# Kernel tuning notes

Hardware: AMD Instinct MI355X
Metric: run time of the kernel (lower is better)

Reference implementation:

```python
import jax, jax.numpy as jnp
import numpy as np

B, S, H = 32, 2048, 1024

def setup_inputs() -> dict:
    key = jax.random.key(0)
    ks = jax.random.split(key, 8)
    scale = 1.0 / np.sqrt(H)
    return {
        "query": jax.random.normal(ks[0], (B, H), jnp.float32),
        "keys": jax.random.normal(ks[1], (B, S, H), jnp.float32),
        "Wa_w": jax.random.uniform(ks[2], (H, H), jnp.float32, -scale, scale),
        "Wa_b": jax.random.uniform(ks[3], (H,), jnp.float32, -scale, scale),
        "Ua_w": jax.random.uniform(ks[4], (H, H), jnp.float32, -scale, scale),
        "Ua_b": jax.random.uniform(ks[5], (H,), jnp.float32, -scale, scale),
        "Va_w": jax.random.uniform(ks[6], (1, H), jnp.float32, -scale, scale),
        "Va_b": jax.random.uniform(ks[7], (1,), jnp.float32, -scale, scale),
    }

def reference(query, keys, Wa_w, Wa_b, Ua_w, Ua_b, Va_w, Va_b):
    # q_proj: [B, H]; k_proj: [B, S, H]  (torch Linear: x @ W^T + b)
    q_proj = query @ Wa_w.T + Wa_b
    k_proj = jnp.einsum("bsh,gh->bsg", keys, Ua_w) + Ua_b
    # scores: [B, S, 1] via thin Va projection of tanh-combined features
    scores = jnp.tanh(q_proj[:, None, :] + k_proj) @ Va_w.T + Va_b
    weights = jax.nn.softmax(scores, axis=1)            # [B, S, 1]
    context = jnp.einsum("bsx,bsh->bxh", weights, keys)  # [B, 1, H]
    return context, weights[:, :, 0]
```

## Files before the change

### kernel.cpp

```cpp
#include <hip/hip_runtime.h>
#include <hip/hip_bf16.h>
#include <stdint.h>

#define B_ 32
#define S_ 2048
#define H_ 1024

typedef __attribute__((ext_vector_type(8))) short short8;
typedef __attribute__((ext_vector_type(4))) float floatx4;

__device__ inline unsigned short f32_bf16(float f) {
    union { float f; unsigned u; } v; v.f = f;
    unsigned u = v.u;
    u += 0x7fff + ((u >> 16) & 1);
    return (unsigned short)(u >> 16);
}

__device__ inline float tanh_fast(float x) {
    float e = __expf(2.0f * x);
    return 1.0f - 2.0f / (e + 1.0f);
}

__global__ void k_zero2(float* a, int na, float* b, int nb) {
    int i = blockIdx.x * 256 + threadIdx.x;
    if (i < na) a[i] = 0.0f;
    else if (i - na < nb) b[i - na] = 0.0f;
}

__global__ void k_cvt_ua(const float* __restrict__ ua, unsigned short* __restrict__ out) {
    int i = (blockIdx.x * 256 + threadIdx.x) * 4;
    float4 f = *(const float4*)(ua + i);
    unsigned lo = f32_bf16(f.x) | ((unsigned)f32_bf16(f.y) << 16);
    unsigned hi = f32_bf16(f.z) | ((unsigned)f32_bf16(f.w) << 16);
    *(uint2*)(out + i) = make_uint2(lo, hi);
}

__global__ void k_qproj(const float* __restrict__ query, const float* __restrict__ Wa_w,
                        const float* __restrict__ Wa_b, const float* __restrict__ Ua_b,
                        float* __restrict__ qsum) {
    int b = blockIdx.x >> 2;
    int g = ((blockIdx.x & 3) << 8) + threadIdx.x;
    const float4* q4 = (const float4*)(query + (size_t)b * H_);
    const float4* w4 = (const float4*)(Wa_w + (size_t)g * H_);
    float acc = 0.0f;
#pragma unroll 4
    for (int h = 0; h < H_ / 4; ++h) {
        float4 a = q4[h], w = w4[h];
        acc += a.x * w.x + a.y * w.y + a.z * w.z + a.w * w.w;
    }
    qsum[b * H_ + g] = acc + Wa_b[g] + Ua_b[g];
}

#define BM 128
#define BN 128
#define BK 32
#define LDA 48

__global__ __launch_bounds__(256, 2) void k_scores(
    const float* __restrict__ keys, const unsigned short* __restrict__ uab,
    const float* __restrict__ qsum, const float* __restrict__ va,
    float* __restrict__ scores)
{
    __shared__ unsigned short Al[BM * LDA];
    __shared__ unsigned short Bl[BN * LDA];

    int bx = blockIdx.x;
    int x  = bx & 7;
    int i  = bx >> 3;
    int tile_m = x * 64 + (i >> 3);
    int nc     = i & 7;
    int m_base = tile_m * BM;
    int b      = m_base >> 11;
    int g0     = nc * BN;

    int tid = threadIdx.x;
    int wid = tid >> 6, lane = tid & 63;
    int wm = wid >> 1, wn = wid & 1;
    int q = lane >> 4, cn = lane & 15;

    const float*          Aptr = keys + (size_t)m_base * H_;
    const unsigned short* Bptr = uab  + (size_t)g0 * H_;

    int ar = tid >> 3;
    int ac = tid & 7;
    int br = tid >> 2;
    int bc = tid & 3;

    floatx4 acc[4][4];
#pragma unroll
    for (int ii = 0; ii < 4; ++ii)
#pragma unroll
        for (int jj = 0; jj < 4; ++jj)
            acc[ii][jj] = (floatx4)(0.0f);

    float4 a0, a1, a2, a3;
    uint4  bv0, bv1;
    {
        int k0 = 0;
        a0 = *(const float4*)(Aptr + (size_t)(ar      ) * H_ + k0 + ac * 4);
        a1 = *(const float4*)(Aptr + (size_t)(ar + 32 ) * H_ + k0 + ac * 4);
        a2 = *(const float4*)(Aptr + (size_t)(ar + 64 ) * H_ + k0 + ac * 4);
        a3 = *(const float4*)(Aptr + (size_t)(ar + 96 ) * H_ + k0 + ac * 4);
        bv0 = *(const uint4*)(Bptr + (size_t)(br      ) * H_ + k0 + bc * 8);
        bv1 = *(const uint4*)(Bptr + (size_t)(br + 64 ) * H_ + k0 + bc * 8);
    }

    for (int kc = 0; kc < H_ / BK; ++kc) {
        __syncthreads();
        {
            unsigned short* p;
            unsigned lo, hi;
            p = Al + (ar      ) * LDA + ac * 4;
            lo = f32_bf16(a0.x) | ((unsigned)f32_bf16(a0.y) << 16);
            hi = f32_bf16(a0.z) | ((unsigned)f32_bf16(a0.w) << 16);
            *(uint2*)p = make_uint2(lo, hi);
            p = Al + (ar + 32 ) * LDA + ac * 4;
            lo = f32_bf16(a1.x) | ((unsigned)f32_bf16(a1.y) << 16);
            hi = f32_bf16(a1.z) | ((unsigned)f32_bf16(a1.w) << 16);
            *(uint2*)p = make_uint2(lo, hi);
            p = Al + (ar + 64 ) * LDA + ac * 4;
            lo = f32_bf16(a2.x) | ((unsigned)f32_bf16(a2.y) << 16);
            hi = f32_bf16(a2.z) | ((unsigned)f32_bf16(a2.w) << 16);
            *(uint2*)p = make_uint2(lo, hi);
            p = Al + (ar + 96 ) * LDA + ac * 4;
            lo = f32_bf16(a3.x) | ((unsigned)f32_bf16(a3.y) << 16);
            hi = f32_bf16(a3.z) | ((unsigned)f32_bf16(a3.w) << 16);
            *(uint2*)p = make_uint2(lo, hi);
            *(uint4*)(Bl + (br      ) * LDA + bc * 8) = bv0;
            *(uint4*)(Bl + (br + 64 ) * LDA + bc * 8) = bv1;
        }
        if (kc + 1 < H_ / BK) {
            int k0 = (kc + 1) * BK;
            a0 = *(const float4*)(Aptr + (size_t)(ar      ) * H_ + k0 + ac * 4);
            a1 = *(const float4*)(Aptr + (size_t)(ar + 32 ) * H_ + k0 + ac * 4);
            a2 = *(const float4*)(Aptr + (size_t)(ar + 64 ) * H_ + k0 + ac * 4);
            a3 = *(const float4*)(Aptr + (size_t)(ar + 96 ) * H_ + k0 + ac * 4);
            bv0 = *(const uint4*)(Bptr + (size_t)(br      ) * H_ + k0 + bc * 8);
            bv1 = *(const uint4*)(Bptr + (size_t)(br + 64 ) * H_ + k0 + bc * 8);
        }
        __syncthreads();
        short8 af[4], bf[4];
#pragma unroll
        for (int ii = 0; ii < 4; ++ii)
            af[ii] = *(const short8*)(Al + (wm * 64 + ii * 16 + cn) * LDA + q * 8);
#pragma unroll
        for (int jj = 0; jj < 4; ++jj)
            bf[jj] = *(const short8*)(Bl + (wn * 64 + jj * 16 + cn) * LDA + q * 8);
#pragma unroll
        for (int ii = 0; ii < 4; ++ii)
#pragma unroll
            for (int jj = 0; jj < 4; ++jj)
                acc[ii][jj] = __builtin_amdgcn_mfma_f32_16x16x32_bf16(
                    af[ii], bf[jj], acc[ii][jj], 0, 0, 0);
    }

    float qs[4], vw[4];
#pragma unroll
    for (int jj = 0; jj < 4; ++jj) {
        int g = g0 + wn * 64 + jj * 16 + cn;
        qs[jj] = qsum[b * H_ + g];
        vw[jj] = va[g];
    }
#pragma unroll
    for (int ii = 0; ii < 4; ++ii) {
        float rs[4] = {0.f, 0.f, 0.f, 0.f};
#pragma unroll
        for (int jj = 0; jj < 4; ++jj) {
#pragma unroll
            for (int r = 0; r < 4; ++r)
                rs[r] += vw[jj] * tanh_fast(qs[jj] + acc[ii][jj][r]);
        }
#pragma unroll
        for (int r = 0; r < 4; ++r) {
            for (int mm = 1; mm < 16; mm <<= 1)
                rs[r] += __shfl_xor(rs[r], mm);
        }
        if (cn == 0) {
            int msrow = m_base + wm * 64 + ii * 16 + q * 4;
            float* sp = scores + b * S_ + (msrow & (S_ - 1));
            atomicAdd(sp + 0, rs[0]);
            atomicAdd(sp + 1, rs[1]);
            atomicAdd(sp + 2, rs[2]);
            atomicAdd(sp + 3, rs[3]);
        }
    }
}

__global__ void k_softmax(const float* __restrict__ scores, float* __restrict__ weights) {
    int b = blockIdx.x;
    int t = threadIdx.x;
    __shared__ float red[4];
    float v[8];
    float mx = -1e30f;
#pragma unroll
    for (int k = 0; k < 8; ++k) { v[k] = scores[b * S_ + t + k * 256]; mx = fmaxf(mx, v[k]); }
    for (int mm = 1; mm < 64; mm <<= 1) mx = fmaxf(mx, __shfl_xor(mx, mm));
    if ((t & 63) == 0) red[t >> 6] = mx;
    __syncthreads();
    mx = fmaxf(fmaxf(red[0], red[1]), fmaxf(red[2], red[3]));
    float sum = 0.0f;
#pragma unroll
    for (int k = 0; k < 8; ++k) { v[k] = __expf(v[k] - mx); sum += v[k]; }
    for (int mm = 1; mm < 64; mm <<= 1) sum += __shfl_xor(sum, mm);
    __syncthreads();
    if ((t & 63) == 0) red[t >> 6] = sum;
    __syncthreads();
    sum = red[0] + red[1] + red[2] + red[3];
    float inv = 1.0f / sum;
#pragma unroll
    for (int k = 0; k < 8; ++k) weights[b * S_ + t + k * 256] = v[k] * inv;
}

__global__ void k_context(const float* __restrict__ keys, const float* __restrict__ weights,
                          float* __restrict__ ctx) {
    int blk = blockIdx.x;
    int b  = blk >> 5;
    int sc = blk & 31;
    int t  = threadIdx.x;
    const float4* kp = (const float4*)(keys + (size_t)(b * S_ + sc * 64) * H_);
    const float*  wp = weights + b * S_ + sc * 64;
    float4 acc = {0.f, 0.f, 0.f, 0.f};
#pragma unroll 4
    for (int s = 0; s < 64; ++s) {
        float w = wp[s];
        float4 k4 = kp[(size_t)s * (H_ / 4) + t];
        acc.x += w * k4.x; acc.y += w * k4.y; acc.z += w * k4.z; acc.w += w * k4.w;
    }
    float* cp = ctx + b * H_ + t * 4;
    atomicAdd(cp + 0, acc.x); atomicAdd(cp + 1, acc.y);
    atomicAdd(cp + 2, acc.z); atomicAdd(cp + 3, acc.w);
}

extern "C" void kernel_launch(void* const* d_in, const int* in_sizes, int n_in,
                              void* d_out, int out_size, void* d_ws, size_t ws_size,
                              hipStream_t stream) {
    const float* query = (const float*)d_in[0];
    const float* keys  = (const float*)d_in[1];
    const float* Wa_w  = (const float*)d_in[2];
    const float* Wa_b  = (const float*)d_in[3];
    const float* Ua_w  = (const float*)d_in[4];
    const float* Ua_b  = (const float*)d_in[5];
    const float* Va_w  = (const float*)d_in[6];

    float* out     = (float*)d_out;
    float* ctx     = out;
    float* weights = out + B_ * H_;

    char* ws = (char*)d_ws;
    unsigned short* uab   = (unsigned short*)ws;
    float*          qsum  = (float*)(ws + 2u * 1024 * 1024);
    float*          scores= (float*)(ws + 2u * 1024 * 1024 + 128 * 1024);

    k_zero2  <<<(B_ * H_ + B_ * S_ + 255) / 256, 256, 0, stream>>>(ctx, B_ * H_, scores, B_ * S_);
    k_cvt_ua <<<(H_ * H_) / 1024, 256, 0, stream>>>(Ua_w, uab);
    k_qproj  <<<B_ * 4, 256, 0, stream>>>(query, Wa_w, Wa_b, Ua_b, qsum);
    k_scores <<<4096, 256, 0, stream>>>(keys, uab, qsum, Va_w, scores);
    k_softmax<<<B_, 256, 0, stream>>>(scores, weights);
    k_context<<<B_ * 16 * 2, 256, 0, stream>>>(keys, weights, ctx);
}
```

Measured before the change: 636.5 us.

## Pre-convert keys to bf16, use direct-to-LDS loads, restructure qproj and context

```diff
diff --git a/kernel.cpp b/kernel.cpp
--- a/kernel.cpp
+++ b/kernel.cpp
@@ -15,54 +15,99 @@
     u += 0x7fff + ((u >> 16) & 1);
     return (unsigned short)(u >> 16);
 }
+__device__ inline unsigned pack_bf2(float a, float b) {
+    return (unsigned)f32_bf16(a) | ((unsigned)f32_bf16(b) << 16);
+}
+__device__ inline float bf_lo(unsigned u) { union { unsigned u; float f; } v; v.u = u << 16; return v.f; }
+__device__ inline float bf_hi(unsigned u) { union { unsigned u; float f; } v; v.u = u & 0xffff0000u; return v.f; }
 
 __device__ inline float tanh_fast(float x) {
     float e = __expf(2.0f * x);
     return 1.0f - 2.0f / (e + 1.0f);
 }
 
-__global__ void k_zero2(float* a, int na, float* b, int nb) {
-    int i = blockIdx.x * 256 + threadIdx.x;
-    if (i < na) a[i] = 0.0f;
-    else if (i - na < nb) b[i - na] = 0.0f;
-}
-
-__global__ void k_cvt_ua(const float* __restrict__ ua, unsigned short* __restrict__ out) {
-    int i = (blockIdx.x * 256 + threadIdx.x) * 4;
-    float4 f = *(const float4*)(ua + i);
-    unsigned lo = f32_bf16(f.x) | ((unsigned)f32_bf16(f.y) << 16);
-    unsigned hi = f32_bf16(f.z) | ((unsigned)f32_bf16(f.w) << 16);
-    *(uint2*)(out + i) = make_uint2(lo, hi);
+__device__ inline void gld16(const void* g, void* l) {
+    __builtin_amdgcn_global_load_lds(
+        (const __attribute__((address_space(1))) unsigned int*)g,
+        (__attribute__((address_space(3))) unsigned int*)l, 16, 0, 0);
+}
+
+#define KCVT_BLOCKS 32768
+#define UACVT_BLOCKS 512
+#define ZS_BLOCKS 64
+__global__ void k_prep(const float* __restrict__ keys, unsigned short* __restrict__ keysbf,
+                       const float* __restrict__ ua, unsigned short* __restrict__ uab,
+                       float* __restrict__ scores) {
+    int blk = blockIdx.x, t = threadIdx.x;
+    if (blk < KCVT_BLOCKS + UACVT_BLOCKS) {
+        const float* src; unsigned short* dst; size_t base;
+        if (blk < KCVT_BLOCKS) { src = keys; dst = keysbf; base = (size_t)blk * 2048; }
+        else { src = ua; dst = uab; base = (size_t)(blk - KCVT_BLOCKS) * 2048; }
+        float4 v0 = *(const float4*)(src + base + t * 4);
+        float4 v1 = *(const float4*)(src + base + 1024 + t * 4);
+        *(uint2*)(dst + base + t * 4)        = make_uint2(pack_bf2(v0.x, v0.y), pack_bf2(v0.z, v0.w));
+        *(uint2*)(dst + base + 1024 + t * 4) = make_uint2(pack_bf2(v1.x, v1.y), pack_bf2(v1.z, v1.w));
+    } else {
+        int zb = blk - KCVT_BLOCKS - UACVT_BLOCKS;
+        float4 z = {0.f, 0.f, 0.f, 0.f};
+        *(float4*)(scores + zb * 1024 + t * 4) = z;
+    }
 }
 
 __global__ void k_qproj(const float* __restrict__ query, const float* __restrict__ Wa_w,
                         const float* __restrict__ Wa_b, const float* __restrict__ Ua_b,
                         float* __restrict__ qsum) {
-    int b = blockIdx.x >> 2;
-    int g = ((blockIdx.x & 3) << 8) + threadIdx.x;
-    const float4* q4 = (const float4*)(query + (size_t)b * H_);
-    const float4* w4 = (const float4*)(Wa_w + (size_t)g * H_);
-    float acc = 0.0f;
-#pragma unroll 4
-    for (int h = 0; h < H_ / 4; ++h) {
-        float4 a = q4[h], w = w4[h];
-        acc += a.x * w.x + a.y * w.y + a.z * w.z + a.w * w.w;
-    }
-    qsum[b * H_ + g] = acc + Wa_b[g] + Ua_b[g];
+    __shared__ float qs_l[32][68];
+    int g0 = blockIdx.x * 16;
+    int t = threadIdx.x;
+    int r = t >> 4;
+    int l = t & 15;
+    int g = g0 + r;
+    float acc[32];
+#pragma unroll
+    for (int b = 0; b < 32; ++b) acc[b] = 0.0f;
+
+    int sb = t >> 3;
+    int sc = (t & 7) * 8;
+    for (int hc = 0; hc < 16; ++hc) {
+        __syncthreads();
+        float4 v0 = *(const float4*)(query + (size_t)sb * H_ + hc * 64 + sc);
+        float4 v1 = *(const float4*)(query + (size_t)sb * H_ + hc * 64 + sc + 4);
+        *(float4*)&qs_l[sb][sc]     = v0;
+        *(float4*)&qs_l[sb][sc + 4] = v1;
+        __syncthreads();
+        float4 w = *(const float4*)(Wa_w + (size_t)g * H_ + hc * 64 + l * 4);
+#pragma unroll
+        for (int b = 0; b < 32; ++b) {
+            float4 q4 = *(const float4*)&qs_l[b][l * 4];
+            acc[b] += w.x * q4.x + w.y * q4.y + w.z * q4.z + w.w * q4.w;
+        }
+    }
+#pragma unroll
+    for (int b = 0; b < 32; ++b) {
+        float a = acc[b];
+        a += __shfl_xor(a, 1); a += __shfl_xor(a, 2);
+        a += __shfl_xor(a, 4); a += __shfl_xor(a, 8);
+        acc[b] = a;
+    }
+    if (l == 0) {
+        float bias = Wa_b[g] + Ua_b[g];
+#pragma unroll
+        for (int b = 0; b < 32; ++b) qsum[b * H_ + g] = acc[b] + bias;
+    }
 }
 
 #define BM 128
 #define BN 128
 #define BK 32
-#define LDA 48
-
-__global__ __launch_bounds__(256, 2) void k_scores(
-    const float* __restrict__ keys, const unsigned short* __restrict__ uab,
+
+__global__ __launch_bounds__(256, 3) void k_scores(
+    const unsigned short* __restrict__ keysbf, const unsigned short* __restrict__ uab,
     const float* __restrict__ qsum, const float* __restrict__ va,
     float* __restrict__ scores)
 {
-    __shared__ unsigned short Al[BM * LDA];
-    __shared__ unsigned short Bl[BN * LDA];
+    __shared__ unsigned short Al[BM * BK];
+    __shared__ unsigned short Bl[BN * BK];
 
     int bx = blockIdx.x;
     int x  = bx & 7;
@@ -78,13 +123,26 @@
     int wm = wid >> 1, wn = wid & 1;
     int q = lane >> 4, cn = lane & 15;
 
-    const float*          Aptr = keys + (size_t)m_base * H_;
-    const unsigned short* Bptr = uab  + (size_t)g0 * H_;
-
-    int ar = tid >> 3;
-    int ac = tid & 7;
-    int br = tid >> 2;
-    int bc = tid & 3;
+    int rl = lane >> 2, cg = lane & 3;
+    int rA0 = wid * 32 + rl,      rA1 = wid * 32 + 16 + rl;
+    int gA0 = cg ^ ((rA0 >> 1) & 3), gA1 = cg ^ ((rA1 >> 1) & 3);
+    const unsigned short* pA0 = keysbf + (size_t)(m_base + rA0) * H_ + gA0 * 8;
+    const unsigned short* pA1 = keysbf + (size_t)(m_base + rA1) * H_ + gA1 * 8;
+    const unsigned short* pB0 = uab + (size_t)(g0 + rA0) * H_ + gA0 * 8;
+    const unsigned short* pB1 = uab + (size_t)(g0 + rA1) * H_ + gA1 * 8;
+    unsigned short* lA0 = &Al[(wid * 32) * BK];
+    unsigned short* lA1 = &Al[(wid * 32 + 16) * BK];
+    unsigned short* lB0 = &Bl[(wid * 32) * BK];
+    unsigned short* lB1 = &Bl[(wid * 32 + 16) * BK];
+
+    int aoff[4], boff[4];
+#pragma unroll
+    for (int ii = 0; ii < 4; ++ii) {
+        int r = wm * 64 + ii * 16 + cn;
+        aoff[ii] = r * BK + (q ^ ((r >> 1) & 3)) * 8;
+        int rb = wn * 64 + ii * 16 + cn;
+        boff[ii] = rb * BK + (q ^ ((rb >> 1) & 3)) * 8;
+    }
 
     floatx4 acc[4][4];
 #pragma unroll
@@ -93,59 +151,19 @@
         for (int jj = 0; jj < 4; ++jj)
             acc[ii][jj] = (floatx4)(0.0f);
 
-    float4 a0, a1, a2, a3;
-    uint4  bv0, bv1;
-    {
-        int k0 = 0;
-        a0 = *(const float4*)(Aptr + (size_t)(ar      ) * H_ + k0 + ac * 4);
-        a1 = *(const float4*)(Aptr + (size_t)(ar + 32 ) * H_ + k0 + ac * 4);
-        a2 = *(const float4*)(Aptr + (size_t)(ar + 64 ) * H_ + k0 + ac * 4);
-        a3 = *(const float4*)(Aptr + (size_t)(ar + 96 ) * H_ + k0 + ac * 4);
-        bv0 = *(const uint4*)(Bptr + (size_t)(br      ) * H_ + k0 + bc * 8);
-        bv1 = *(const uint4*)(Bptr + (size_t)(br + 64 ) * H_ + k0 + bc * 8);
-    }
-
     for (int kc = 0; kc < H_ / BK; ++kc) {
         __syncthreads();
-        {
-            unsigned short* p;
-            unsigned lo, hi;
-            p = Al + (ar      ) * LDA + ac * 4;
-            lo = f32_bf16(a0.x) | ((unsigned)f32_bf16(a0.y) << 16);
-            hi = f32_bf16(a0.z) | ((unsigned)f32_bf16(a0.w) << 16);
-            *(uint2*)p = make_uint2(lo, hi);
-            p = Al + (ar + 32 ) * LDA + ac * 4;
-            lo = f32_bf16(a1.x) | ((unsigned)f32_bf16(a1.y) << 16);
-            hi = f32_bf16(a1.z) | ((unsigned)f32_bf16(a1.w) << 16);
-            *(uint2*)p = make_uint2(lo, hi);
-            p = Al + (ar + 64 ) * LDA + ac * 4;
-            lo = f32_bf16(a2.x) | ((unsigned)f32_bf16(a2.y) << 16);
-            hi = f32_bf16(a2.z) | ((unsigned)f32_bf16(a2.w) << 16);
-            *(uint2*)p = make_uint2(lo, hi);
-            p = Al + (ar + 96 ) * LDA + ac * 4;
-            lo = f32_bf16(a3.x) | ((unsigned)f32_bf16(a3.y) << 16);
-            hi = f32_bf16(a3.z) | ((unsigned)f32_bf16(a3.w) << 16);
-            *(uint2*)p = make_uint2(lo, hi);
-            *(uint4*)(Bl + (br      ) * LDA + bc * 8) = bv0;
-            *(uint4*)(Bl + (br + 64 ) * LDA + bc * 8) = bv1;
-        }
-        if (kc + 1 < H_ / BK) {
-            int k0 = (kc + 1) * BK;
-            a0 = *(const float4*)(Aptr + (size_t)(ar      ) * H_ + k0 + ac * 4);
-            a1 = *(const float4*)(Aptr + (size_t)(ar + 32 ) * H_ + k0 + ac * 4);
-            a2 = *(const float4*)(Aptr + (size_t)(ar + 64 ) * H_ + k0 + ac * 4);
-            a3 = *(const float4*)(Aptr + (size_t)(ar + 96 ) * H_ + k0 + ac * 4);
-            bv0 = *(const uint4*)(Bptr + (size_t)(br      ) * H_ + k0 + bc * 8);
-            bv1 = *(const uint4*)(Bptr + (size_t)(br + 64 ) * H_ + k0 + bc * 8);
-        }
+        int ko = kc * BK;
+        gld16(pA0 + ko, lA0);
+        gld16(pA1 + ko, lA1);
+        gld16(pB0 + ko, lB0);
+        gld16(pB1 + ko, lB1);
         __syncthreads();
         short8 af[4], bf[4];
 #pragma unroll
-        for (int ii = 0; ii < 4; ++ii)
-            af[ii] = *(const short8*)(Al + (wm * 64 + ii * 16 + cn) * LDA + q * 8);
-#pragma unroll
-        for (int jj = 0; jj < 4; ++jj)
-            bf[jj] = *(const short8*)(Bl + (wn * 64 + jj * 16 + cn) * LDA + q * 8);
+        for (int ii = 0; ii < 4; ++ii) af[ii] = *(const short8*)&Al[aoff[ii]];
+#pragma unroll
+        for (int jj = 0; jj < 4; ++jj) bf[jj] = *(const short8*)&Bl[boff[jj]];
 #pragma unroll
         for (int ii = 0; ii < 4; ++ii)
 #pragma unroll
@@ -211,24 +229,43 @@
     for (int k = 0; k < 8; ++k) weights[b * S_ + t + k * 256] = v[k] * inv;
 }
 
-__global__ void k_context(const float* __restrict__ keys, const float* __restrict__ weights,
-                          float* __restrict__ ctx) {
+__global__ void k_ctx1(const unsigned short* __restrict__ keysbf,
+                       const float* __restrict__ weights, float* __restrict__ partial) {
     int blk = blockIdx.x;
-    int b  = blk >> 5;
-    int sc = blk & 31;
-    int t  = threadIdx.x;
-    const float4* kp = (const float4*)(keys + (size_t)(b * S_ + sc * 64) * H_);
-    const float*  wp = weights + b * S_ + sc * 64;
-    float4 acc = {0.f, 0.f, 0.f, 0.f};
-#pragma unroll 4
-    for (int s = 0; s < 64; ++s) {
-        float w = wp[s];
-        float4 k4 = kp[(size_t)s * (H_ / 4) + t];
-        acc.x += w * k4.x; acc.y += w * k4.y; acc.z += w * k4.z; acc.w += w * k4.w;
-    }
-    float* cp = ctx + b * H_ + t * 4;
-    atomicAdd(cp + 0, acc.x); atomicAdd(cp + 1, acc.y);
-    atomicAdd(cp + 2, acc.z); atomicAdd(cp + 3, acc.w);
+    int b = blk >> 5, sc = blk & 31;
+    int t = threadIdx.x;
+    __shared__ float wl[64];
+    if (t < 64) wl[t] = weights[b * S_ + sc * 64 + t];
+    __syncthreads();
+    const uint4* kp = (const uint4*)(keysbf + (size_t)(b * S_ + sc * 64) * H_);
+    int col = t & 127;
+    int rp  = t >> 7;
+    float a0=0,a1=0,a2=0,a3=0,a4=0,a5=0,a6=0,a7=0;
+#pragma unroll 8
+    for (int s = rp; s < 64; s += 2) {
+        uint4 v = kp[(size_t)s * 128 + col];
+        float w = wl[s];
+        a0 += w * bf_lo(v.x); a1 += w * bf_hi(v.x);
+        a2 += w * bf_lo(v.y); a3 += w * bf_hi(v.y);
+        a4 += w * bf_lo(v.z); a5 += w * bf_hi(v.z);
+        a6 += w * bf_lo(v.w); a7 += w * bf_hi(v.w);
+    }
+    float* pp = partial + (size_t)(b * 64 + sc * 2 + rp) * H_ + col * 8;
+    float4 o0 = {a0, a1, a2, a3}, o1 = {a4, a5, a6, a7};
+    *(float4*)pp = o0;
+    *(float4*)(pp + 4) = o1;
+}
+
+__global__ void k_ctx2(const float* __restrict__ partial, float* __restrict__ ctx) {
+    int b = blockIdx.x;
+    int t = threadIdx.x;
+    float4 a = {0.f, 0.f, 0.f, 0.f};
+#pragma unroll 8
+    for (int j = 0; j < 64; ++j) {
+        float4 p = *(const float4*)(partial + (size_t)(b * 64 + j) * H_ + t * 4);
+        a.x += p.x; a.y += p.y; a.z += p.z; a.w += p.w;
+    }
+    *(float4*)(ctx + b * H_ + t * 4) = a;
 }
 
 extern "C" void kernel_launch(void* const* d_in, const int* in_sizes, int n_in,
@@ -247,14 +284,16 @@
     float* weights = out + B_ * H_;
 
     char* ws = (char*)d_ws;
-    unsigned short* uab   = (unsigned short*)ws;
-    float*          qsum  = (float*)(ws + 2u * 1024 * 1024);
-    float*          scores= (float*)(ws + 2u * 1024 * 1024 + 128 * 1024);
-
-    k_zero2  <<<(B_ * H_ + B_ * S_ + 255) / 256, 256, 0, stream>>>(ctx, B_ * H_, scores, B_ * S_);
-    k_cvt_ua <<<(H_ * H_) / 1024, 256, 0, stream>>>(Ua_w, uab);
-    k_qproj  <<<B_ * 4, 256, 0, stream>>>(query, Wa_w, Wa_b, Ua_b, qsum);
-    k_scores <<<4096, 256, 0, stream>>>(keys, uab, qsum, Va_w, scores);
+    unsigned short* keysbf = (unsigned short*)ws;
+    unsigned short* uab    = (unsigned short*)(ws + 134217728);
+    float*          qsum   = (float*)(ws + 134217728 + 2097152);
+    float*          scores = (float*)(ws + 134217728 + 2097152 + 131072);
+    float*          partial= (float*)(ws + 134217728 + 2097152 + 131072 + 262144);
+
+    k_prep   <<<KCVT_BLOCKS + UACVT_BLOCKS + ZS_BLOCKS, 256, 0, stream>>>(keys, keysbf, Ua_w, uab, scores);
+    k_qproj  <<<64, 256, 0, stream>>>(query, Wa_w, Wa_b, Ua_b, qsum);
+    k_scores <<<4096, 256, 0, stream>>>(keysbf, uab, qsum, Va_w, scores);
     k_softmax<<<B_, 256, 0, stream>>>(scores, weights);
-    k_context<<<B_ * 16 * 2, 256, 0, stream>>>(keys, weights, ctx);
-}
+    k_ctx1   <<<B_ * 32, 256, 0, stream>>>(keysbf, weights, partial);
+    k_ctx2   <<<B_, 256, 0, stream>>>(partial, ctx);
+}
```

New measurement: 627.7 us. About the same (-1.4%).
